# Optimization experiments

Measured on AMD Instinct MI355X. Metric: run time of the kernel, lower is better.

Reference implementation:

```python
import jax, jax.numpy as jnp
import numpy as np

INV_TEMP = 20.0
THRESHOLD = 0.01
EPS = 1e-12


def setup_inputs() -> dict:
    key = jax.random.key(0)
    k1, k2, k3, k4, k5 = jax.random.split(key, 5)
    B, NA, NB, D, K = 1, 4096, 4096, 256, 8
    return {
        "keypoints_A": jax.random.uniform(k1, (B, NA, 2), jnp.float32) * 2.0 - 1.0,
        "descriptions_A": jax.random.normal(k2, (B, NA, D), jnp.float32),
        "keypoints_B": jax.random.uniform(k3, (B, NB, 2), jnp.float32) * 2.0 - 1.0,
        "descriptions_B": jax.random.normal(k4, (B, NB, D), jnp.float32),
        # steerer prototype affine maps: one DxD matrix per prototype, scaled to
        # keep steered descriptors at unit-ish norm (acts like ~orthogonal map)
        "prototype_mats": jax.random.normal(k5, (K, D, D), jnp.float32) / np.float32(np.sqrt(D)),
    }


def _neg_dist_similarity(a, b):
    # negative Euclidean distance, matching -torch.cdist(a, b)
    a2 = jnp.sum(a * a, axis=-1)[..., :, None]   # [B, NA, 1]
    b2 = jnp.sum(b * b, axis=-1)[..., None, :]   # [B, 1, NB]
    d2 = jnp.maximum(a2 + b2 - 2.0 * jnp.einsum('bnd,bmd->bnm', a, b), 0.0)
    return -jnp.sqrt(d2 + EPS)                   # [B, NA, NB]


def reference(keypoints_A, descriptions_A, keypoints_B, descriptions_B, prototype_mats):
    # base similarity
    corr = _neg_dist_similarity(descriptions_A, descriptions_B)  # [B, NA, NB]

    # looped augmented-similarity max-accumulate (one pass per prototype affine)
    def step(c, M):
        dA_aug = jnp.einsum('bnd,ed->bne', descriptions_A, M)  # steered descriptors
        return jnp.maximum(c, _neg_dist_similarity(dA_aug, descriptions_B)), None

    corr, _ = jax.lax.scan(step, corr, prototype_mats)

    corr = INV_TEMP * corr
    # dual softmax matching
    P = jax.nn.softmax(corr, axis=-2) * jax.nn.softmax(corr, axis=-1)  # [B, NA, NB]

    # mutual nearest neighbour + threshold (fixed-shape boolean mask instead of nonzero)
    mask = (P == P.max(axis=-1, keepdims=True)) \
         & (P == P.max(axis=-2, keepdims=True)) \
         & (P > THRESHOLD)

    # fixed-shape match extraction: best B-index per A keypoint + validity flag
    j = jnp.argmax(P, axis=-1)                                   # [B, NA]
    valid = jnp.take_along_axis(mask, j[..., None], axis=-1)[..., 0]  # [B, NA]
    matches_B = jnp.take_along_axis(keypoints_B, j[..., None], axis=1)  # [B, NA, 2]
    return P, mask, valid, matches_B
```

## Files before the change

### kernel.cpp

```cpp
#include <hip/hip_runtime.h>
#include <math.h>

#define NPT 4096
#define DIM 256
#define NVAR 9
#define INV_TEMP 20.0f
#define THR 0.01f
#define EPSD 1e-12f

typedef unsigned short u16;
typedef __attribute__((ext_vector_type(8))) __bf16 bf16x8;
typedef __attribute__((ext_vector_type(4))) float f32x4;

__device__ __forceinline__ unsigned frep(float x) {
    unsigned u = __float_as_uint(x);
    return (u & 0x80000000u) ? ~u : (u | 0x80000000u);
}
__device__ __forceinline__ float funrep(unsigned u) {
    return __uint_as_float((u & 0x80000000u) ? (u ^ 0x80000000u) : ~u);
}

__device__ __forceinline__ u16 f2bf(float x) {
    unsigned u = __float_as_uint(x);
    u += 0x7fffu + ((u >> 16) & 1u);
    return (u16)(u >> 16);
}
__device__ __forceinline__ float bf2f(u16 h) {
    return __uint_as_float(((unsigned)h) << 16);
}
__device__ __forceinline__ void split_hl(float x, u16& h, u16& l) {
    u16 hh = f2bf(x);
    h = hh;
    l = f2bf(x - bf2f(hh));
}

__device__ __forceinline__ void gl_lds16(const void* g, void* l) {
    __builtin_amdgcn_global_load_lds(
        (const __attribute__((address_space(1))) void*)g,
        (__attribute__((address_space(3))) void*)l, 16, 0, 0);
}

#define NA4 (NPT * DIM / 4)
#define NP4 (8 * DIM * DIM / 4)
__global__ __launch_bounds__(256) void conv3_kernel(const float* __restrict__ A,
                                                    const float* __restrict__ B,
                                                    const float* __restrict__ Pr,
                                                    u16* __restrict__ Ahi, u16* __restrict__ Alo,
                                                    u16* __restrict__ Bhi, u16* __restrict__ Blo,
                                                    u16* __restrict__ Phi, u16* __restrict__ Plo) {
    int i = blockIdx.x * 256 + threadIdx.x;
    const float* src;
    u16 *dh, *dl;
    int j;
    if (i < NA4) { src = A; dh = Ahi; dl = Alo; j = i; }
    else if (i < 2 * NA4) { src = B; dh = Bhi; dl = Blo; j = i - NA4; }
    else if (i < 2 * NA4 + NP4) { src = Pr; dh = Phi; dl = Plo; j = i - 2 * NA4; }
    else return;
    float4 v = ((const float4*)src)[j];
    ushort4 h, l;
    split_hl(v.x, h.x, l.x);
    split_hl(v.y, h.y, l.y);
    split_hl(v.z, h.z, l.z);
    split_hl(v.w, h.w, l.w);
    ((ushort4*)dh)[j] = h;
    ((ushort4*)dl)[j] = l;
}

__global__ __launch_bounds__(256, 2) void steer_mfma_kernel(
    const u16* __restrict__ A0h, const u16* __restrict__ A0l,
    const u16* __restrict__ Ph, const u16* __restrict__ Pl,
    u16* __restrict__ outH, u16* __restrict__ outL) {
    __shared__ u16 lds[32768];
    u16* LAh = lds;
    u16* LAl = lds + 8192;
    u16* LBh = lds + 16384;
    u16* LBl = lds + 24576;

    const int tid = threadIdx.x, lane = tid & 63, wave = tid >> 6;
    const int l15 = lane & 15, lg = lane >> 4;
    const int wr = (wave >> 1) * 64, wc = (wave & 1) * 64;
    const int rb = blockIdx.x * 128;
    const int eb = blockIdx.y * 128;
    const int k = blockIdx.z;
    const u16* Bh_g = Ph + (size_t)k * DIM * DIM;
    const u16* Bl_g = Pl + (size_t)k * DIM * DIM;
    const int s_row = tid >> 3;
    const int s_ch = tid & 7;
    const int s_gch = s_ch ^ (s_row & 7);
    const int c0 = lg ^ (l15 & 7);

    f32x4 acc[4][4];
#pragma unroll
    for (int m = 0; m < 4; ++m)
#pragma unroll
        for (int n = 0; n < 4; ++n) acc[m][n] = 0.0f;

    for (int kb = 0; kb < 4; ++kb) {
        const int k0 = kb * 64;
        __syncthreads();
#pragma unroll
        for (int r = 0; r < 4; ++r) {
            int row = r * 32 + s_row;
            size_t ga = (size_t)(rb + row) * DIM + k0 + s_gch * 8;
            size_t gb = (size_t)(eb + row) * DIM + k0 + s_gch * 8;
            int lo = row * 64 + s_ch * 8;
            gl_lds16(A0h + ga, &LAh[lo]);
            gl_lds16(A0l + ga, &LAl[lo]);
            gl_lds16(Bh_g + gb, &LBh[lo]);
            gl_lds16(Bl_g + gb, &LBl[lo]);
        }
        __syncthreads();
#pragma unroll
        for (int ks = 0; ks < 2; ++ks) {
            const int cx = (c0 ^ (ks << 2)) * 8;
            bf16x8 ah[4], al[4], bh[4], bl[4];
#pragma unroll
            for (int m = 0; m < 4; ++m) {
                int ro = (wr + m * 16 + l15) * 64 + cx;
                ah[m] = *(const bf16x8*)&LAh[ro];
                al[m] = *(const bf16x8*)&LAl[ro];
            }
#pragma unroll
            for (int n = 0; n < 4; ++n) {
                int ro = (wc + n * 16 + l15) * 64 + cx;
                bh[n] = *(const bf16x8*)&LBh[ro];
                bl[n] = *(const bf16x8*)&LBl[ro];
            }
#pragma unroll
            for (int m = 0; m < 4; ++m)
#pragma unroll
                for (int n = 0; n < 4; ++n)
                    acc[m][n] = __builtin_amdgcn_mfma_f32_16x16x32_bf16(ah[m], bh[n], acc[m][n], 0, 0, 0);
#pragma unroll
            for (int m = 0; m < 4; ++m)
#pragma unroll
                for (int n = 0; n < 4; ++n)
                    acc[m][n] = __builtin_amdgcn_mfma_f32_16x16x32_bf16(al[m], bh[n], acc[m][n], 0, 0, 0);
#pragma unroll
            for (int m = 0; m < 4; ++m)
#pragma unroll
                for (int n = 0; n < 4; ++n)
                    acc[m][n] = __builtin_amdgcn_mfma_f32_16x16x32_bf16(ah[m], bl[n], acc[m][n], 0, 0, 0);
        }
    }
#pragma unroll
    for (int m = 0; m < 4; ++m)
#pragma unroll
        for (int j = 0; j < 4; ++j) {
            size_t row = (size_t)(k + 1) * NPT + rb + wr + m * 16 + lg * 4 + j;
#pragma unroll
            for (int n = 0; n < 4; ++n) {
                u16 h, l;
                split_hl(acc[m][n][j], h, l);
                size_t idx = row * DIM + eb + wc + n * 16 + l15;
                outH[idx] = h;
                outL[idx] = l;
            }
        }
}

__global__ __launch_bounds__(256) void rownorm10_kernel(const u16* __restrict__ AH,
                                                        const u16* __restrict__ AL,
                                                        const u16* __restrict__ BH,
                                                        const u16* __restrict__ BL,
                                                        float* __restrict__ out) {
    int w = blockIdx.x * 4 + (threadIdx.x >> 6);
    int lane = threadIdx.x & 63;
    const u16 *H, *L;
    size_t row;
    if (w < NVAR * NPT) { H = AH; L = AL; row = w; }
    else { H = BH; L = BL; row = w - NVAR * NPT; }
    ushort4 h = *(const ushort4*)&H[row * DIM + lane * 4];
    ushort4 l = *(const ushort4*)&L[row * DIM + lane * 4];
    float x0 = bf2f(h.x) + bf2f(l.x);
    float x1 = bf2f(h.y) + bf2f(l.y);
    float x2 = bf2f(h.z) + bf2f(l.z);
    float x3 = bf2f(h.w) + bf2f(l.w);
    float s = x0 * x0 + x1 * x1 + x2 * x2 + x3 * x3;
#pragma unroll
    for (int o = 32; o; o >>= 1) s += __shfl_xor(s, o);
    if (lane == 0) out[w] = s;
}

__global__ __launch_bounds__(256, 2) void corr_mfma_kernel(
    const u16* __restrict__ Ahi, const u16* __restrict__ Alo,
    const u16* __restrict__ Bhi, const u16* __restrict__ Blo,
    const float* __restrict__ a2, const float* __restrict__ b2,
    float* __restrict__ cOut, unsigned* __restrict__ rm_rep, unsigned* __restrict__ cm_rep) {
    __shared__ u16 lds[32768];
    u16* LAh = lds;
    u16* LAl = lds + 8192;
    u16* LBh = lds + 16384;
    u16* LBl = lds + 24576;

    const int tid = threadIdx.x, lane = tid & 63, wave = tid >> 6;
    const int l15 = lane & 15, lg = lane >> 4;
    const int wr = (wave >> 1) * 64, wc = (wave & 1) * 64;
    int wg = blockIdx.y * 32 + blockIdx.x;
    wg = (wg & 7) * 128 + (wg >> 3);
    const int rb = (wg >> 5) * 128;
    const int cb = (wg & 31) * 128;
    const int s_row = tid >> 3;
    const int s_ch = tid & 7;
    const int s_gch = s_ch ^ (s_row & 7);
    const int c0 = lg ^ (l15 & 7);

    float b2c[4];
#pragma unroll
    for (int n = 0; n < 4; ++n) b2c[n] = b2[cb + wc + n * 16 + l15];

    f32x4 zmin[4][4];
#pragma unroll
    for (int m = 0; m < 4; ++m)
#pragma unroll
        for (int n = 0; n < 4; ++n) zmin[m][n] = 3.402823466e38f;

    for (int v = 0; v < NVAR; ++v) {
        const u16* Ah_g = Ahi + (size_t)v * NPT * DIM;
        const u16* Al_g = Alo + (size_t)v * NPT * DIM;
        f32x4 acc[4][4];
#pragma unroll
        for (int m = 0; m < 4; ++m)
#pragma unroll
            for (int n = 0; n < 4; ++n) acc[m][n] = 0.0f;

        for (int kb = 0; kb < 4; ++kb) {
            const int k0 = kb * 64;
            __syncthreads();
#pragma unroll
            for (int r = 0; r < 4; ++r) {
                int row = r * 32 + s_row;
                size_t ga = (size_t)(rb + row) * DIM + k0 + s_gch * 8;
                size_t gb = (size_t)(cb + row) * DIM + k0 + s_gch * 8;
                int lo = row * 64 + s_ch * 8;
                gl_lds16(Ah_g + ga, &LAh[lo]);
                gl_lds16(Al_g + ga, &LAl[lo]);
                gl_lds16(Bhi + gb, &LBh[lo]);
                gl_lds16(Blo + gb, &LBl[lo]);
            }
            __syncthreads();
#pragma unroll
            for (int ks = 0; ks < 2; ++ks) {
                const int cx = (c0 ^ (ks << 2)) * 8;
                bf16x8 ah[4], al[4], bh[4], bl[4];
#pragma unroll
                for (int m = 0; m < 4; ++m) {
                    int ro = (wr + m * 16 + l15) * 64 + cx;
                    ah[m] = *(const bf16x8*)&LAh[ro];
                    al[m] = *(const bf16x8*)&LAl[ro];
                }
#pragma unroll
                for (int n = 0; n < 4; ++n) {
                    int ro = (wc + n * 16 + l15) * 64 + cx;
                    bh[n] = *(const bf16x8*)&LBh[ro];
                    bl[n] = *(const bf16x8*)&LBl[ro];
                }
#pragma unroll
                for (int m = 0; m < 4; ++m)
#pragma unroll
                    for (int n = 0; n < 4; ++n)
                        acc[m][n] = __builtin_amdgcn_mfma_f32_16x16x32_bf16(ah[m], bh[n], acc[m][n], 0, 0, 0);
#pragma unroll
                for (int m = 0; m < 4; ++m)
#pragma unroll
                    for (int n = 0; n < 4; ++n)
                        acc[m][n] = __builtin_amdgcn_mfma_f32_16x16x32_bf16(al[m], bh[n], acc[m][n], 0, 0, 0);
#pragma unroll
                for (int m = 0; m < 4; ++m)
#pragma unroll
                    for (int n = 0; n < 4; ++n)
                        acc[m][n] = __builtin_amdgcn_mfma_f32_16x16x32_bf16(ah[m], bl[n], acc[m][n], 0, 0, 0);
            }
        }
#pragma unroll
        for (int m = 0; m < 4; ++m) {
            float4 a4 = *(const float4*)&a2[(size_t)v * NPT + rb + wr + m * 16 + lg * 4];
            const float* a4p = (const float*)&a4;
#pragma unroll
            for (int n = 0; n < 4; ++n)
#pragma unroll
                for (int j = 0; j < 4; ++j) {
                    float d2 = fmaxf(a4p[j] + b2c[n] - 2.0f * acc[m][n][j], 0.0f);
                    zmin[m][n][j] = fminf(zmin[m][n][j], d2);
                }
        }
    }

    unsigned* redR = (unsigned*)lds;
    unsigned* redC = (unsigned*)(lds + 8192);
    __syncthreads();
    if (tid < 128) { redR[tid] = 0u; redC[tid] = 0u; }
    __syncthreads();

    float colmax[4] = {-3.402823466e38f, -3.402823466e38f, -3.402823466e38f, -3.402823466e38f};
#pragma unroll
    for (int m = 0; m < 4; ++m) {
#pragma unroll
        for (int j = 0; j < 4; ++j) {
            int row = rb + wr + m * 16 + lg * 4 + j;
            float rmax = -3.402823466e38f;
#pragma unroll
            for (int n = 0; n < 4; ++n) {
                float c = -INV_TEMP * sqrtf(zmin[m][n][j] + EPSD);
                cOut[(size_t)row * NPT + cb + wc + n * 16 + l15] = c;
                rmax = fmaxf(rmax, c);
                colmax[n] = fmaxf(colmax[n], c);
            }
            atomicMax(&redR[wr + m * 16 + lg * 4 + j], frep(rmax));
        }
    }
#pragma unroll
    for (int n = 0; n < 4; ++n)
        atomicMax(&redC[wc + n * 16 + l15], frep(colmax[n]));
    __syncthreads();
    if (tid < 128) {
        atomicMax(&rm_rep[rb + tid], redR[tid]);
        atomicMax(&cm_rep[cb + tid], redC[tid]);
    }
}


__global__ __launch_bounds__(256) void sums_kernel(const float* __restrict__ C,
                                                   const unsigned* __restrict__ rm_rep,
                                                   const unsigned* __restrict__ cm_rep,
                                                   float* __restrict__ rowsum,
                                                   float* __restrict__ colsum) {
    const int tid = threadIdx.x, lane = tid & 63, wv = tid >> 6;
    const int c0 = (blockIdx.x & 15) * 256;
    const int r0 = (blockIdx.x >> 4) * 64;
    const int colq = (c0 >> 2) + lane;
    __shared__ float rmbuf[64];
    __shared__ float cred[4][256];
    if (tid < 64) rmbuf[tid] = funrep(rm_rep[r0 + tid]);
    uint4 cmr = ((const uint4*)cm_rep)[colq];
    float cm0 = funrep(cmr.x), cm1 = funrep(cmr.y), cm2 = funrep(cmr.z), cm3 = funrep(cmr.w);
    __syncthreads();
    float4 csa = make_float4(0.f, 0.f, 0.f, 0.f);
#pragma unroll
    for (int it = 0; it < 16; ++it) {
        int r = r0 + it * 4 + wv;
        float4 cv = ((const float4*)C)[(size_t)r * (NPT / 4) + colq];
        float rm = rmbuf[it * 4 + wv];
        float er = expf(cv.x - rm) + expf(cv.y - rm) + expf(cv.z - rm) + expf(cv.w - rm);
#pragma unroll
        for (int o = 32; o; o >>= 1) er += __shfl_xor(er, o);
        if (lane == 0) atomicAdd(&rowsum[r], er);
        csa.x += expf(cv.x - cm0);
        csa.y += expf(cv.y - cm1);
        csa.z += expf(cv.z - cm2);
        csa.w += expf(cv.w - cm3);
    }
    cred[wv][lane * 4 + 0] = csa.x;
    cred[wv][lane * 4 + 1] = csa.y;
    cred[wv][lane * 4 + 2] = csa.z;
    cred[wv][lane * 4 + 3] = csa.w;
    __syncthreads();
    float s = (cred[0][tid] + cred[1][tid]) + (cred[2][tid] + cred[3][tid]);
    atomicAdd(&colsum[c0 + tid], s);
}

__global__ __launch_bounds__(256) void pmax_kernel(float* __restrict__ C,
                                                   const unsigned* __restrict__ rm_rep,
                                                   const unsigned* __restrict__ cm_rep,
                                                   const float* __restrict__ rowsum,
                                                   const float* __restrict__ colsum,
                                                   unsigned* __restrict__ rmp_rep,
                                                   unsigned* __restrict__ cmp_rep) {
    const int tid = threadIdx.x, lane = tid & 63, wv = tid >> 6;
    const int c0 = (blockIdx.x & 15) * 256;
    const int r0 = (blockIdx.x >> 4) * 64;
    const int colq = (c0 >> 2) + lane;
    __shared__ float rmbuf[64], rsbuf[64];
    __shared__ float cred[4][256];
    if (tid < 64) {
        rmbuf[tid] = funrep(rm_rep[r0 + tid]);
        rsbuf[tid] = rowsum[r0 + tid];
    }
    uint4 cmr = ((const uint4*)cm_rep)[colq];
    float cm0 = funrep(cmr.x), cm1 = funrep(cmr.y), cm2 = funrep(cmr.z), cm3 = funrep(cmr.w);
    float4 csv = ((const float4*)colsum)[colq];
    __syncthreads();
    float4 cmax = make_float4(-1.f, -1.f, -1.f, -1.f);
#pragma unroll
    for (int it = 0; it < 16; ++it) {
        int r = r0 + it * 4 + wv;
        size_t idx = (size_t)r * (NPT / 4) + colq;
        float4 cv = ((const float4*)C)[idx];
        float rm = rmbuf[it * 4 + wv];
        float rs = rsbuf[it * 4 + wv];
        float4 p;
        p.x = (expf(cv.x - cm0) / csv.x) * (expf(cv.x - rm) / rs);
        p.y = (expf(cv.y - cm1) / csv.y) * (expf(cv.y - rm) / rs);
        p.z = (expf(cv.z - cm2) / csv.z) * (expf(cv.z - rm) / rs);
        p.w = (expf(cv.w - cm3) / csv.w) * (expf(cv.w - rm) / rs);
        ((float4*)C)[idx] = p;
        float pm = fmaxf(fmaxf(p.x, p.y), fmaxf(p.z, p.w));
#pragma unroll
        for (int o = 32; o; o >>= 1) pm = fmaxf(pm, __shfl_xor(pm, o));
        if (lane == 0) atomicMax(&rmp_rep[r], frep(pm));
        cmax.x = fmaxf(cmax.x, p.x);
        cmax.y = fmaxf(cmax.y, p.y);
        cmax.z = fmaxf(cmax.z, p.z);
        cmax.w = fmaxf(cmax.w, p.w);
    }
    cred[wv][lane * 4 + 0] = cmax.x;
    cred[wv][lane * 4 + 1] = cmax.y;
    cred[wv][lane * 4 + 2] = cmax.z;
    cred[wv][lane * 4 + 3] = cmax.w;
    __syncthreads();
    float m = fmaxf(fmaxf(cred[0][tid], cred[1][tid]), fmaxf(cred[2][tid], cred[3][tid]));
    atomicMax(&cmp_rep[c0 + tid], frep(m));
}

__global__ __launch_bounds__(256) void maskarg_kernel(const float* __restrict__ P,
                                                      const unsigned* __restrict__ rmp_rep,
                                                      const unsigned* __restrict__ cmp_rep,
                                                      float* __restrict__ maskOut,
                                                      int* __restrict__ argJ) {
    const int tid = threadIdx.x, lane = tid & 63, wv = tid >> 6;
    const int c0 = (blockIdx.x & 15) * 256;
    const int r0 = (blockIdx.x >> 4) * 64;
    const int colq = (c0 >> 2) + lane;
    const int col4 = c0 + lane * 4;
    __shared__ float rpbuf[64];
    if (tid < 64) rpbuf[tid] = funrep(rmp_rep[r0 + tid]);
    uint4 cpr = ((const uint4*)cmp_rep)[colq];
    float cp0 = funrep(cpr.x), cp1 = funrep(cpr.y), cp2 = funrep(cpr.z), cp3 = funrep(cpr.w);
    __syncthreads();
#pragma unroll
    for (int it = 0; it < 16; ++it) {
        int r = r0 + it * 4 + wv;
        size_t idx = (size_t)r * (NPT / 4) + colq;
        float4 p = ((const float4*)P)[idx];
        float rmp = rpbuf[it * 4 + wv];
        float4 m;
        m.x = (p.x == rmp && p.x == cp0 && p.x > THR) ? 1.f : 0.f;
        m.y = (p.y == rmp && p.y == cp1 && p.y > THR) ? 1.f : 0.f;
        m.z = (p.z == rmp && p.z == cp2 && p.z > THR) ? 1.f : 0.f;
        m.w = (p.w == rmp && p.w == cp3 && p.w > THR) ? 1.f : 0.f;
        ((float4*)maskOut)[idx] = m;
        int cand = 0x7fffffff;
        if (p.w == rmp) cand = col4 + 3;
        if (p.z == rmp) cand = col4 + 2;
        if (p.y == rmp) cand = col4 + 1;
        if (p.x == rmp) cand = col4 + 0;
#pragma unroll
        for (int o = 32; o; o >>= 1) cand = min(cand, __shfl_xor(cand, o));
        if (lane == 0) atomicMin(&argJ[r], cand);
    }
}

__global__ __launch_bounds__(256) void valid_kernel(const float* __restrict__ P,
                                                    const unsigned* __restrict__ cmp_rep,
                                                    const int* __restrict__ argJ,
                                                    const float* __restrict__ kpB,
                                                    float* __restrict__ validOut,
                                                    float* __restrict__ matchOut) {
    int n = blockIdx.x * 256 + threadIdx.x;
    int j = argJ[n];
    float pj = P[(size_t)n * NPT + j];
    bool v = (pj == funrep(cmp_rep[j])) && (pj > THR);
    validOut[n] = v ? 1.f : 0.f;
    matchOut[2 * n + 0] = kpB[2 * j + 0];
    matchOut[2 * n + 1] = kpB[2 * j + 1];
}

extern "C" void kernel_launch(void* const* d_in, const int* in_sizes, int n_in,
                              void* d_out, int out_size, void* d_ws, size_t ws_size,
                              hipStream_t stream) {
    const float* dA     = (const float*)d_in[1];
    const float* kpB    = (const float*)d_in[2];
    const float* dB     = (const float*)d_in[3];
    const float* protos = (const float*)d_in[4];

    float* P      = (float*)d_out;
    float* maskO  = P + (size_t)NPT * NPT;
    float* validO = maskO + (size_t)NPT * NPT;
    float* matchO = validO + NPT;

    u16* Ahi = (u16*)maskO;
    u16* Alo = Ahi + (size_t)NVAR * NPT * DIM;
    u16* Bhi = Alo + (size_t)NVAR * NPT * DIM;
    u16* Blo = Bhi + (size_t)NPT * DIM;
    u16* Phi = Blo + (size_t)NPT * DIM;
    u16* Plo = Phi + (size_t)8 * DIM * DIM;

    float* ws      = (float*)d_ws;
    float* a2      = ws;
    float* b2      = a2 + NVAR * NPT;
    unsigned* rm   = (unsigned*)(b2 + NPT);
    unsigned* cm   = rm + NPT;
    float* rs      = (float*)(cm + NPT);
    float* cs      = rs + NPT;
    unsigned* rmp  = (unsigned*)(cs + NPT);
    unsigned* cmp  = rmp + NPT;
    int* argJ      = (int*)(cmp + NPT);

    hipMemsetAsync(rm, 0, 6 * NPT * sizeof(unsigned), stream);
    hipMemsetAsync(argJ, 0x7f, NPT * sizeof(int), stream);

    conv3_kernel<<<2560, 256, 0, stream>>>(dA, dB, protos, Ahi, Alo, Bhi, Blo, Phi, Plo);
    steer_mfma_kernel<<<dim3(32, 2, 8), 256, 0, stream>>>(Ahi, Alo, Phi, Plo, Ahi, Alo);
    rownorm10_kernel<<<(NVAR + 1) * NPT / 4, 256, 0, stream>>>(Ahi, Alo, Bhi, Blo, a2);
    corr_mfma_kernel<<<dim3(32, 32), 256, 0, stream>>>(Ahi, Alo, Bhi, Blo, a2, b2, P, rm, cm);
    sums_kernel<<<1024, 256, 0, stream>>>(P, rm, cm, rs, cs);
    pmax_kernel<<<1024, 256, 0, stream>>>(P, rm, cm, rs, cs, rmp, cmp);
    maskarg_kernel<<<1024, 256, 0, stream>>>(P, rmp, cmp, maskO, argJ);
    valid_kernel<<<16, 256, 0, stream>>>(P, cmp, argJ, kpB, validO, matchO);
}
```

Measured before the change: 429.7 us.

## Fuse online softmax partial sums into corr kernel and reduce atomics via LDS

The corr kernel now computes per-tile partial row and column max and exp-sum values and writes them out. A small combine kernel rescales and merges these partials into the row and column sums, which removes the separate sums_kernel pass over the 64MB correlation matrix. The pmax kernel folds the two softmax exps into one __expf with precomputed reciprocals. Both pmax and maskarg replace per-row shuffle reductions plus global atomics with LDS transposed reductions. The trade-off is extra epilogue work and register pressure in the GEMM kernel, plus fast-math exp that could change exact equality comparisons against P.

```diff
diff --git a/kernel.cpp b/kernel.cpp
--- a/kernel.cpp
+++ b/kernel.cpp
@@ -186,7 +186,9 @@
     const u16* __restrict__ Ahi, const u16* __restrict__ Alo,
     const u16* __restrict__ Bhi, const u16* __restrict__ Blo,
     const float* __restrict__ a2, const float* __restrict__ b2,
-    float* __restrict__ cOut, unsigned* __restrict__ rm_rep, unsigned* __restrict__ cm_rep) {
+    float* __restrict__ cOut, unsigned* __restrict__ rm_rep, unsigned* __restrict__ cm_rep,
+    float* __restrict__ pMaxR, float* __restrict__ pSumR,
+    float* __restrict__ pMaxC, float* __restrict__ pSumC) {
     __shared__ u16 lds[32768];
     u16* LAh = lds;
     u16* LAl = lds + 8192;
@@ -200,6 +202,7 @@
     wg = (wg & 7) * 128 + (wg >> 3);
     const int rb = (wg >> 5) * 128;
     const int cb = (wg & 31) * 128;
+    const int rbIdx = rb >> 7, cbIdx = cb >> 7;
     const int s_row = tid >> 3;
     const int s_ch = tid & 7;
     const int s_gch = s_ch ^ (s_row & 7);
@@ -287,9 +290,11 @@
     }
 
     unsigned* redR = (unsigned*)lds;
-    unsigned* redC = (unsigned*)(lds + 8192);
-    __syncthreads();
-    if (tid < 128) { redR[tid] = 0u; redC[tid] = 0u; }
+    unsigned* redC = redR + 128;
+    float* bsumR = (float*)(redC + 128);
+    float* bsumC = bsumR + 128;
+    __syncthreads();
+    if (tid < 128) { redR[tid] = 0u; redC[tid] = 0u; bsumR[tid] = 0.f; bsumC[tid] = 0.f; }
     __syncthreads();
 
     float colmax[4] = {-3.402823466e38f, -3.402823466e38f, -3.402823466e38f, -3.402823466e38f};
@@ -313,51 +318,80 @@
     for (int n = 0; n < 4; ++n)
         atomicMax(&redC[wc + n * 16 + l15], frep(colmax[n]));
     __syncthreads();
+
+    float bmc[4], colS[4];
+#pragma unroll
+    for (int n = 0; n < 4; ++n) {
+        bmc[n] = funrep(redC[wc + n * 16 + l15]);
+        colS[n] = 0.f;
+    }
+#pragma unroll
+    for (int m = 0; m < 4; ++m) {
+#pragma unroll
+        for (int j = 0; j < 4; ++j) {
+            int lr = wr + m * 16 + lg * 4 + j;
+            float bm = funrep(redR[lr]);
+            float s = 0.f;
+#pragma unroll
+            for (int n = 0; n < 4; ++n) {
+                float c = -INV_TEMP * sqrtf(zmin[m][n][j] + EPSD);
+                s += __expf(c - bm);
+                colS[n] += __expf(c - bmc[n]);
+            }
+            s += __shfl_xor(s, 1);
+            s += __shfl_xor(s, 2);
+            s += __shfl_xor(s, 4);
+            s += __shfl_xor(s, 8);
+            if (l15 == 0) atomicAdd(&bsumR[lr], s);
+        }
+    }
+#pragma unroll
+    for (int n = 0; n < 4; ++n) {
+        float s = colS[n];
+        s += __shfl_xor(s, 16);
+        s += __shfl_xor(s, 32);
+        if (lg == 0) atomicAdd(&bsumC[wc + n * 16 + l15], s);
+    }
+    __syncthreads();
+
     if (tid < 128) {
         atomicMax(&rm_rep[rb + tid], redR[tid]);
-        atomicMax(&cm_rep[cb + tid], redC[tid]);
-    }
-}
-
-
-__global__ __launch_bounds__(256) void sums_kernel(const float* __restrict__ C,
-                                                   const unsigned* __restrict__ rm_rep,
-                                                   const unsigned* __restrict__ cm_rep,
-                                                   float* __restrict__ rowsum,
-                                                   float* __restrict__ colsum) {
-    const int tid = threadIdx.x, lane = tid & 63, wv = tid >> 6;
-    const int c0 = (blockIdx.x & 15) * 256;
-    const int r0 = (blockIdx.x >> 4) * 64;
-    const int colq = (c0 >> 2) + lane;
-    __shared__ float rmbuf[64];
-    __shared__ float cred[4][256];
-    if (tid < 64) rmbuf[tid] = funrep(rm_rep[r0 + tid]);
-    uint4 cmr = ((const uint4*)cm_rep)[colq];
-    float cm0 = funrep(cmr.x), cm1 = funrep(cmr.y), cm2 = funrep(cmr.z), cm3 = funrep(cmr.w);
-    __syncthreads();
-    float4 csa = make_float4(0.f, 0.f, 0.f, 0.f);
-#pragma unroll
-    for (int it = 0; it < 16; ++it) {
-        int r = r0 + it * 4 + wv;
-        float4 cv = ((const float4*)C)[(size_t)r * (NPT / 4) + colq];
-        float rm = rmbuf[it * 4 + wv];
-        float er = expf(cv.x - rm) + expf(cv.y - rm) + expf(cv.z - rm) + expf(cv.w - rm);
-#pragma unroll
-        for (int o = 32; o; o >>= 1) er += __shfl_xor(er, o);
-        if (lane == 0) atomicAdd(&rowsum[r], er);
-        csa.x += expf(cv.x - cm0);
-        csa.y += expf(cv.y - cm1);
-        csa.z += expf(cv.z - cm2);
-        csa.w += expf(cv.w - cm3);
-    }
-    cred[wv][lane * 4 + 0] = csa.x;
-    cred[wv][lane * 4 + 1] = csa.y;
-    cred[wv][lane * 4 + 2] = csa.z;
-    cred[wv][lane * 4 + 3] = csa.w;
-    __syncthreads();
-    float s = (cred[0][tid] + cred[1][tid]) + (cred[2][tid] + cred[3][tid]);
-    atomicAdd(&colsum[c0 + tid], s);
-}
+        pMaxR[(size_t)cbIdx * NPT + rb + tid] = funrep(redR[tid]);
+        pSumR[(size_t)cbIdx * NPT + rb + tid] = bsumR[tid];
+    } else {
+        int t = tid - 128;
+        atomicMax(&cm_rep[cb + t], redC[t]);
+        pMaxC[(size_t)rbIdx * NPT + cb + t] = funrep(redC[t]);
+        pSumC[(size_t)rbIdx * NPT + cb + t] = bsumC[t];
+    }
+}
+
+__global__ __launch_bounds__(256) void combine_kernel(const unsigned* __restrict__ rm_rep,
+                                                      const unsigned* __restrict__ cm_rep,
+                                                      const float* __restrict__ pMaxR,
+                                                      const float* __restrict__ pSumR,
+                                                      const float* __restrict__ pMaxC,
+                                                      const float* __restrict__ pSumC,
+                                                      float* __restrict__ rowsum,
+                                                      float* __restrict__ colsum) {
+    int idx = (blockIdx.x & 15) * 256 + threadIdx.x;
+    if (blockIdx.x < 16) {
+        float gm = funrep(rm_rep[idx]);
+        float s = 0.f;
+#pragma unroll
+        for (int b = 0; b < 32; ++b)
+            s += pSumR[(size_t)b * NPT + idx] * __expf(pMaxR[(size_t)b * NPT + idx] - gm);
+        rowsum[idx] = s;
+    } else {
+        float gm = funrep(cm_rep[idx]);
+        float s = 0.f;
+#pragma unroll
+        for (int b = 0; b < 32; ++b)
+            s += pSumC[(size_t)b * NPT + idx] * __expf(pMaxC[(size_t)b * NPT + idx] - gm);
+        colsum[idx] = s;
+    }
+}
+
 
 __global__ __launch_bounds__(256) void pmax_kernel(float* __restrict__ C,
                                                    const unsigned* __restrict__ rm_rep,
@@ -370,34 +404,35 @@
     const int c0 = (blockIdx.x & 15) * 256;
     const int r0 = (blockIdx.x >> 4) * 64;
     const int colq = (c0 >> 2) + lane;
-    __shared__ float rmbuf[64], rsbuf[64];
+    __shared__ float rmbuf[64], rrbuf[64];
+    __shared__ float pmLds[64 * 65];
+    __shared__ float qred[256];
     __shared__ float cred[4][256];
     if (tid < 64) {
         rmbuf[tid] = funrep(rm_rep[r0 + tid]);
-        rsbuf[tid] = rowsum[r0 + tid];
+        rrbuf[tid] = 1.0f / rowsum[r0 + tid];
     }
     uint4 cmr = ((const uint4*)cm_rep)[colq];
     float cm0 = funrep(cmr.x), cm1 = funrep(cmr.y), cm2 = funrep(cmr.z), cm3 = funrep(cmr.w);
     float4 csv = ((const float4*)colsum)[colq];
+    float rc0 = 1.0f / csv.x, rc1 = 1.0f / csv.y, rc2 = 1.0f / csv.z, rc3 = 1.0f / csv.w;
     __syncthreads();
     float4 cmax = make_float4(-1.f, -1.f, -1.f, -1.f);
 #pragma unroll
     for (int it = 0; it < 16; ++it) {
-        int r = r0 + it * 4 + wv;
+        int lr = it * 4 + wv;
+        int r = r0 + lr;
         size_t idx = (size_t)r * (NPT / 4) + colq;
         float4 cv = ((const float4*)C)[idx];
-        float rm = rmbuf[it * 4 + wv];
-        float rs = rsbuf[it * 4 + wv];
+        float rm = rmbuf[lr];
+        float rr = rrbuf[lr];
         float4 p;
-        p.x = (expf(cv.x - cm0) / csv.x) * (expf(cv.x - rm) / rs);
-        p.y = (expf(cv.y - cm1) / csv.y) * (expf(cv.y - rm) / rs);
-        p.z = (expf(cv.z - cm2) / csv.z) * (expf(cv.z - rm) / rs);
-        p.w = (expf(cv.w - cm3) / csv.w) * (expf(cv.w - rm) / rs);
+        p.x = __expf(2.0f * cv.x - cm0 - rm) * (rc0 * rr);
+        p.y = __expf(2.0f * cv.y - cm1 - rm) * (rc1 * rr);
+        p.z = __expf(2.0f * cv.z - cm2 - rm) * (rc2 * rr);
+        p.w = __expf(2.0f * cv.w - cm3 - rm) * (rc3 * rr);
         ((float4*)C)[idx] = p;
-        float pm = fmaxf(fmaxf(p.x, p.y), fmaxf(p.z, p.w));
-#pragma unroll
-        for (int o = 32; o; o >>= 1) pm = fmaxf(pm, __shfl_xor(pm, o));
-        if (lane == 0) atomicMax(&rmp_rep[r], frep(pm));
+        pmLds[lr * 65 + lane] = fmaxf(fmaxf(p.x, p.y), fmaxf(p.z, p.w));
         cmax.x = fmaxf(cmax.x, p.x);
         cmax.y = fmaxf(cmax.y, p.y);
         cmax.z = fmaxf(cmax.z, p.z);
@@ -408,8 +443,21 @@
     cred[wv][lane * 4 + 2] = cmax.z;
     cred[wv][lane * 4 + 3] = cmax.w;
     __syncthreads();
-    float m = fmaxf(fmaxf(cred[0][tid], cred[1][tid]), fmaxf(cred[2][tid], cred[3][tid]));
-    atomicMax(&cmp_rep[c0 + tid], frep(m));
+    {
+        int row = tid & 63, q = tid >> 6;
+        float m = -1.f;
+#pragma unroll
+        for (int i = 0; i < 16; ++i) m = fmaxf(m, pmLds[row * 65 + q * 16 + i]);
+        qred[row * 4 + q] = m;
+    }
+    float mc = fmaxf(fmaxf(cred[0][tid], cred[1][tid]), fmaxf(cred[2][tid], cred[3][tid]));
+    atomicMax(&cmp_rep[c0 + tid], frep(mc));
+    __syncthreads();
+    if (tid < 64) {
+        float m = fmaxf(fmaxf(qred[tid * 4 + 0], qred[tid * 4 + 1]),
+                        fmaxf(qred[tid * 4 + 2], qred[tid * 4 + 3]));
+        atomicMax(&rmp_rep[r0 + tid], frep(m));
+    }
 }
 
 __global__ __launch_bounds__(256) void maskarg_kernel(const float* __restrict__ P,
@@ -423,16 +471,19 @@
     const int colq = (c0 >> 2) + lane;
     const int col4 = c0 + lane * 4;
     __shared__ float rpbuf[64];
+    __shared__ int candLds[64 * 65];
+    __shared__ int qredi[256];
     if (tid < 64) rpbuf[tid] = funrep(rmp_rep[r0 + tid]);
     uint4 cpr = ((const uint4*)cmp_rep)[colq];
     float cp0 = funrep(cpr.x), cp1 = funrep(cpr.y), cp2 = funrep(cpr.z), cp3 = funrep(cpr.w);
     __syncthreads();
 #pragma unroll
     for (int it = 0; it < 16; ++it) {
-        int r = r0 + it * 4 + wv;
+        int lr = it * 4 + wv;
+        int r = r0 + lr;
         size_t idx = (size_t)r * (NPT / 4) + colq;
         float4 p = ((const float4*)P)[idx];
-        float rmp = rpbuf[it * 4 + wv];
+        float rmp = rpbuf[lr];
         float4 m;
         m.x = (p.x == rmp && p.x == cp0 && p.x > THR) ? 1.f : 0.f;
         m.y = (p.y == rmp && p.y == cp1 && p.y > THR) ? 1.f : 0.f;
@@ -444,9 +495,21 @@
         if (p.z == rmp) cand = col4 + 2;
         if (p.y == rmp) cand = col4 + 1;
         if (p.x == rmp) cand = col4 + 0;
-#pragma unroll
-        for (int o = 32; o; o >>= 1) cand = min(cand, __shfl_xor(cand, o));
-        if (lane == 0) atomicMin(&argJ[r], cand);
+        candLds[lr * 65 + lane] = cand;
+    }
+    __syncthreads();
+    {
+        int row = tid & 63, q = tid >> 6;
+        int m = 0x7fffffff;
+#pragma unroll
+        for (int i = 0; i < 16; ++i) m = min(m, candLds[row * 65 + q * 16 + i]);
+        qredi[row * 4 + q] = m;
+    }
+    __syncthreads();
+    if (tid < 64) {
+        int m = min(min(qredi[tid * 4 + 0], qredi[tid * 4 + 1]),
+                    min(qredi[tid * 4 + 2], qredi[tid * 4 + 3]));
+        atomicMin(&argJ[r0 + tid], m);
     }
 }
 
@@ -484,26 +547,31 @@
     u16* Blo = Bhi + (size_t)NPT * DIM;
     u16* Phi = Blo + (size_t)NPT * DIM;
     u16* Plo = Phi + (size_t)8 * DIM * DIM;
+    float* pMaxR = (float*)(Plo + (size_t)8 * DIM * DIM);
+    float* pSumR = pMaxR + 32 * NPT;
+    float* pMaxC = pSumR + 32 * NPT;
+    float* pSumC = pMaxC + 32 * NPT;
 
     float* ws      = (float*)d_ws;
     float* a2      = ws;
     float* b2      = a2 + NVAR * NPT;
     unsigned* rm   = (unsigned*)(b2 + NPT);
     unsigned* cm   = rm + NPT;
-    float* rs      = (float*)(cm + NPT);
+    unsigned* rmp  = cm + NPT;
+    unsigned* cmp  = rmp + NPT;
+    float* rs      = (float*)(cmp + NPT);
     float* cs      = rs + NPT;
-    unsigned* rmp  = (unsigned*)(cs + NPT);
-    unsigned* cmp  = rmp + NPT;
-    int* argJ      = (int*)(cmp + NPT);
-
-    hipMemsetAsync(rm, 0, 6 * NPT * sizeof(unsigned), stream);
+    int* argJ      = (int*)(cs + NPT);
+
+    hipMemsetAsync(rm, 0, 4 * NPT * sizeof(unsigned), stream);
     hipMemsetAsync(argJ, 0x7f, NPT * sizeof(int), stream);
 
     conv3_kernel<<<2560, 256, 0, stream>>>(dA, dB, protos, Ahi, Alo, Bhi, Blo, Phi, Plo);
     steer_mfma_kernel<<<dim3(32, 2, 8), 256, 0, stream>>>(Ahi, Alo, Phi, Plo, Ahi, Alo);
     rownorm10_kernel<<<(NVAR + 1) * NPT / 4, 256, 0, stream>>>(Ahi, Alo, Bhi, Blo, a2);
-    corr_mfma_kernel<<<dim3(32, 32), 256, 0, stream>>>(Ahi, Alo, Bhi, Blo, a2, b2, P, rm, cm);
-    sums_kernel<<<1024, 256, 0, stream>>>(P, rm, cm, rs, cs);
+    corr_mfma_kernel<<<dim3(32, 32), 256, 0, stream>>>(Ahi, Alo, Bhi, Blo, a2, b2, P, rm, cm,
+                                                       pMaxR, pSumR, pMaxC, pSumC);
+    combine_kernel<<<32, 256, 0, stream>>>(rm, cm, pMaxR, pSumR, pMaxC, pSumC, rs, cs);
     pmax_kernel<<<1024, 256, 0, stream>>>(P, rm, cm, rs, cs, rmp, cmp);
     maskarg_kernel<<<1024, 256, 0, stream>>>(P, rmp, cmp, maskO, argJ);
     valid_kernel<<<16, 256, 0, stream>>>(P, cmp, argJ, kpB, validO, matchO);
```

Result: faster. 408.9 us (-4.9%).
